# Kernel tuning notes

Measured on AMD Instinct MI355X. Metric: run time of the kernel, lower is better.

The kernel has to match this reference:

```python
import jax, jax.numpy as jnp
import numpy as np
import math

S, B, H, NH = 2048, 1, 4096, 32
D = H // NH  # 128 head dim


def rotate_half(x):
    x1, x2 = x[..., : x.shape[-1] // 2], x[..., x.shape[-1] // 2 :]
    return jnp.concatenate((-x2, x1), axis=-1)


def setup_inputs() -> dict:
    key = jax.random.key(0)
    k1, k2, k3, k4, k5 = jax.random.split(key, 5)
    hidden_states = jax.random.normal(k1, (S, B, H), dtype=jnp.float32)
    position_ids = jnp.broadcast_to(jnp.arange(S, dtype=jnp.int32)[None, :], (B, S))
    # causal mask: True = masked (upper triangle above diagonal)
    attention_mask = jnp.triu(jnp.ones((S, S), dtype=bool), k=1)[None, None]
    W_qkv = jax.random.normal(k2, (H, 3 * H), dtype=jnp.float32) * 0.02
    b_qkv = jax.random.normal(k3, (3 * H,), dtype=jnp.float32) * 0.02
    W_dense = jax.random.normal(k4, (H, H), dtype=jnp.float32) * 0.02
    b_dense = jax.random.normal(k5, (H,), dtype=jnp.float32) * 0.02
    return {
        "hidden_states": hidden_states,
        "position_ids": position_ids,
        "attention_mask": attention_mask,
        "W_qkv": W_qkv,
        "b_qkv": b_qkv,
        "W_dense": W_dense,
        "b_dense": b_dense,
        "layer_id": 27,
    }


def reference(hidden_states, position_ids, attention_mask, W_qkv, b_qkv, W_dense, b_dense, layer_id):
    s, b, h = hidden_states.shape
    nh, d = NH, D
    # QKV projection: [s, b, 3h] -> [s, b, nh, 3d] -> split
    mixed = hidden_states @ W_qkv + b_qkv
    mixed = mixed.reshape(s, b, nh, 3 * d)
    q, k, v = jnp.split(mixed, 3, axis=-1)  # each [s, b, nh, d]
    # rotary embedding indexed by position_ids (transposed to [s, b])
    pos = position_ids.T  # [s, b]
    inv_freq = 1.0 / (10000.0 ** (jnp.arange(0, d, 2, dtype=jnp.float32) / d))
    freqs = pos[..., None].astype(jnp.float32) * inv_freq  # [s, b, d/2]
    emb = jnp.concatenate((freqs, freqs), axis=-1)  # [s, b, d]
    cos = jnp.cos(emb)[:, :, None, :]  # [s, b, 1, d]
    sin = jnp.sin(emb)[:, :, None, :]
    q = q * cos + rotate_half(q) * sin
    k = k * cos + rotate_half(k) * sin
    # attention with per-layer scaling coeff (cancels in softmax except mask fill)
    coeff = jnp.float32(layer_id + 1)
    q_scaled = q / (math.sqrt(d) * coeff)
    scores = jnp.einsum("sbnd,tbnd->bnst", q_scaled, k)  # [b, nh, s, s]
    scores = jnp.where(attention_mask, jnp.float32(-10000.0), scores) * coeff
    probs = jax.nn.softmax(scores, axis=-1)
    ctx = jnp.einsum("bnst,tbnd->sbnd", probs, v).reshape(s, b, h)
    out = ctx @ W_dense + b_dense
    return out
```

## Files before the change

### kernel.cpp

```cpp
#include <hip/hip_runtime.h>

#define S_LEN 2048
#define HID   4096
#define NHEAD 32
#define DHEAD 128
#define H3    12288

typedef __attribute__((ext_vector_type(8))) __bf16 bf16x8;
typedef __attribute__((ext_vector_type(4))) __bf16 bf16x4;
typedef __attribute__((ext_vector_type(4))) float  f32x4;
typedef __attribute__((ext_vector_type(16))) float f32x16;

__device__ __forceinline__ void gl_lds16(const void* g, void* l) {
  __builtin_amdgcn_global_load_lds(
      (const __attribute__((address_space(1))) void*)g,
      (__attribute__((address_space(3))) void*)l, 16, 0, 0);
}

__global__ void cvt_f32_bf16(const float* __restrict__ in, __bf16* __restrict__ out, int n4) {
  int i = blockIdx.x * blockDim.x + threadIdx.x;
  if (i >= n4) return;
  float4 v = ((const float4*)in)[i];
  bf16x4 o;
  o.x = (__bf16)v.x; o.y = (__bf16)v.y; o.z = (__bf16)v.z; o.w = (__bf16)v.w;
  ((bf16x4*)out)[i] = o;
}

__global__ void transpose_cvt(const float* __restrict__ in, __bf16* __restrict__ out, int R, int C) {
  __shared__ float t[64][65];
  const int tid = threadIdx.x;
  const int r0 = blockIdx.y * 64, c0 = blockIdx.x * 64;
#pragma unroll
  for (int p = 0; p < 4; ++p) {
    int r = p * 16 + (tid >> 4);
    int c4 = (tid & 15) * 4;
    float4 v = *(const float4*)(in + (size_t)(r0 + r) * C + c0 + c4);
    t[r][c4] = v.x; t[r][c4 + 1] = v.y; t[r][c4 + 2] = v.z; t[r][c4 + 3] = v.w;
  }
  __syncthreads();
#pragma unroll
  for (int p = 0; p < 4; ++p) {
    int c = p * 16 + (tid >> 4);
    int rg = (tid & 15) * 4;
    bf16x4 o;
    o.x = (__bf16)t[rg][c]; o.y = (__bf16)t[rg + 1][c];
    o.z = (__bf16)t[rg + 2][c]; o.w = (__bf16)t[rg + 3][c];
    *(bf16x4*)(out + (size_t)(c0 + c) * R + r0 + rg) = o;
  }
}

__global__ void rope_kernel(__bf16* __restrict__ q, __bf16* __restrict__ k,
                            const int* __restrict__ pos) {
  int idx = blockIdx.x * 256 + threadIdx.x;
  int j = idx & 63;
  int hs = idx >> 6;
  int s = hs & (S_LEN - 1);
  float p = (float)pos[s];
  float invf = __expf(-(float)j * (9.210340371976184f / 64.f));
  float a = p * invf;
  float c, sn;
  __sincosf(a, &sn, &c);
  const float SC = 0.08838834764831845f;
  size_t base = (size_t)hs * 128;
  float x1 = (float)q[base + j], x2 = (float)q[base + j + 64];
  q[base + j]      = (__bf16)((x1 * c - x2 * sn) * SC);
  q[base + j + 64] = (__bf16)((x2 * c + x1 * sn) * SC);
  x1 = (float)k[base + j]; x2 = (float)k[base + j + 64];
  k[base + j]      = (__bf16)(x1 * c - x2 * sn);
  k[base + j + 64] = (__bf16)(x2 * c + x1 * sn);
}

__global__ __launch_bounds__(256, 2)
void gemm_dense(const __bf16* __restrict__ A, const __bf16* __restrict__ BT,
                const float* __restrict__ bias, int K,
                float* __restrict__ outf) {
  const int tid = threadIdx.x;
  const int lane = tid & 63;
  const int wave = tid >> 6;
  const int bm = blockIdx.x * 128;
  const int bn = blockIdx.y * 128;

  __shared__ char lds[2][32768];

  f32x4 acc[4][4] = {};

  const int wm = (wave >> 1) * 64;
  const int wn = (wave & 1) * 64;

  const int sr = tid >> 3;
  const int sc = (tid & 7) * 16;
  const int scs = sc ^ ((sr & 7) << 4);

  const char* Arow = (const char*)(A + (size_t)(bm + sr) * K) + scs;
  const char* Brow = (const char*)(BT + (size_t)(bn + sr) * K) + scs;

  const int NT = K >> 6;

  auto stage = [&](int t) {
    const char* a_src = Arow + (size_t)t * 128;
    const char* b_src = Brow + (size_t)t * 128;
    char* a_dst = lds[t & 1] + wave * 1024;
    char* b_dst = lds[t & 1] + 16384 + wave * 1024;
#pragma unroll
    for (int i = 0; i < 4; ++i) {
      gl_lds16(a_src + (size_t)i * 32 * K * 2, a_dst + i * 4096);
      gl_lds16(b_src + (size_t)i * 32 * K * 2, b_dst + i * 4096);
    }
  };

  stage(0);
  __syncthreads();
  for (int t = 0; t < NT; ++t) {
    if (t + 1 < NT) stage(t + 1);
    const char* Ab = lds[t & 1];
    const char* Bb = lds[t & 1] + 16384;
#pragma unroll
    for (int kk = 0; kk < 2; ++kk) {
      bf16x8 af[4], bfr[4];
#pragma unroll
      for (int m = 0; m < 4; ++m) {
        int row = wm + m * 16 + (lane & 15);
        int cb = (kk * 64 + ((lane >> 4) << 4)) ^ ((row & 7) << 4);
        af[m] = *(const bf16x8*)(Ab + row * 128 + cb);
      }
#pragma unroll
      for (int n = 0; n < 4; ++n) {
        int row = wn + n * 16 + (lane & 15);
        int cb = (kk * 64 + ((lane >> 4) << 4)) ^ ((row & 7) << 4);
        bfr[n] = *(const bf16x8*)(Bb + row * 128 + cb);
      }
#pragma unroll
      for (int m = 0; m < 4; ++m)
#pragma unroll
        for (int n = 0; n < 4; ++n)
          acc[m][n] = __builtin_amdgcn_mfma_f32_16x16x32_bf16(af[m], bfr[n], acc[m][n], 0, 0, 0);
    }
    __syncthreads();
  }

  const int rbase = (lane >> 4) << 2;
  const int cl = lane & 15;
#pragma unroll
  for (int n = 0; n < 4; ++n) {
    const int col = bn + wn + n * 16 + cl;
    const float bv = bias[col];
#pragma unroll
    for (int m = 0; m < 4; ++m) {
      const int srow = bm + wm + m * 16 + rbase;
#pragma unroll
      for (int r = 0; r < 4; ++r)
        outf[(size_t)(srow + r) * HID + col] = acc[m][n][r] + bv;
    }
  }
}

template <int EPI>
__global__ __launch_bounds__(256, 2)
void gemm32(const __bf16* __restrict__ A, const __bf16* __restrict__ BT,
            const float* __restrict__ bias, int K,
            __bf16* __restrict__ outq, __bf16* __restrict__ outk,
            __bf16* __restrict__ outvt) {
  const int tid = threadIdx.x;
  const int lane = tid & 63;
  const int wave = tid >> 6;
  const int bm = blockIdx.x * 256;
  const int bn = blockIdx.y * 128;

  __shared__ char lds[49152];
  char* Ab = lds;
  char* Bb = lds + 32768;

  f32x16 acc[4][2] = {};

  const int wm = (wave >> 1) * 128;
  const int wn = (wave & 1) * 64;
  const int l31 = lane & 31;
  const int hi = lane >> 5;

  const int sr = tid >> 3;
  const int scb = ((tid & 7) * 16) ^ ((sr & 7) << 4);
  const int K2 = K * 2;
  const char* Arow = (const char*)A + (size_t)(bm + sr) * K2 + scb;
  const char* Brow = (const char*)BT + (size_t)(bn + sr) * K2 + scb;

  for (int k0 = 0; k0 < K; k0 += 64) {
    const char* a_src = Arow + (size_t)k0 * 2;
    const char* b_src = Brow + (size_t)k0 * 2;
    char* a_dst = Ab + wave * 1024;
    char* b_dst = Bb + wave * 1024;
#pragma unroll
    for (int i = 0; i < 8; ++i)
      gl_lds16(a_src + (size_t)i * 32 * K2, a_dst + i * 4096);
#pragma unroll
    for (int i = 0; i < 4; ++i)
      gl_lds16(b_src + (size_t)i * 32 * K2, b_dst + i * 4096);
    __syncthreads();
#pragma unroll
    for (int kk = 0; kk < 4; ++kk) {
      const int cbase = kk * 32 + (hi << 4);
      bf16x8 af[4], bfr[2];
#pragma unroll
      for (int m = 0; m < 4; ++m) {
        const int row = wm + m * 32 + l31;
        af[m] = *(const bf16x8*)(Ab + row * 128 + (cbase ^ ((row & 7) << 4)));
      }
#pragma unroll
      for (int n = 0; n < 2; ++n) {
        const int row = wn + n * 32 + l31;
        bfr[n] = *(const bf16x8*)(Bb + row * 128 + (cbase ^ ((row & 7) << 4)));
      }
#pragma unroll
      for (int m = 0; m < 4; ++m)
#pragma unroll
        for (int n = 0; n < 2; ++n)
          acc[m][n] = __builtin_amdgcn_mfma_f32_32x32x16_bf16(af[m], bfr[n], acc[m][n], 0, 0, 0);
    }
    __syncthreads();
  }

  const int route = (bn >> 7) % 3;
  const int head = bn / 384;
#pragma unroll
  for (int n = 0; n < 2; ++n) {
    const int d = wn + n * 32 + l31;
    const float bv = bias[bn + d];
#pragma unroll
    for (int m = 0; m < 4; ++m) {
      if (route == 2) {
#pragma unroll
        for (int qd = 0; qd < 4; ++qd) {
          const int srow = bm + wm + m * 32 + qd * 8 + (hi << 2);
          bf16x4 o;
          o.x = (__bf16)(acc[m][n][qd * 4 + 0] + bv);
          o.y = (__bf16)(acc[m][n][qd * 4 + 1] + bv);
          o.z = (__bf16)(acc[m][n][qd * 4 + 2] + bv);
          o.w = (__bf16)(acc[m][n][qd * 4 + 3] + bv);
          *(bf16x4*)(outvt + ((size_t)head * 128 + d) * S_LEN + srow) = o;
        }
      } else {
        __bf16* dst = (route == 0 ? outq : outk) + (size_t)head * S_LEN * 128;
#pragma unroll
        for (int r = 0; r < 16; ++r) {
          const int srow = bm + wm + m * 32 + (r & 3) + 8 * (r >> 2) + (hi << 2);
          dst[(size_t)srow * 128 + d] = (__bf16)(acc[m][n][r] + bv);
        }
      }
    }
  }
}

__global__ __launch_bounds__(256, 2)
void attn_kernel(const __bf16* __restrict__ q, const __bf16* __restrict__ k,
                 const __bf16* __restrict__ vt, __bf16* __restrict__ ctx) {
  const int p = blockIdx.x, h = blockIdx.y;
  const int tid = threadIdx.x, lane = tid & 63, wave = tid >> 6;
  __shared__ char Kd[2][16384];
  __shared__ char Vd[2][16384];
  __shared__ __bf16 Ps[4][16 * 64];
  char* Pb = (char*)(Ps[wave]);

  const __bf16* qh = q + (size_t)h * S_LEN * 128;
  const __bf16* kh = k + (size_t)h * S_LEN * 128;
  const __bf16* vh = vt + (size_t)h * 128 * S_LEN;

  const int cl = lane & 15, rbase = (lane >> 4) << 2;

  const int krow = tid >> 4, kcol = (tid & 15) * 16;
  const int kcs = kcol ^ ((krow & 7) << 4);
  const int vrow = tid >> 3, vcol = (tid & 7) * 16;
  const int vcs = vcol ^ ((vrow & 7) << 4);

  auto stage_kv = [&](int j) {
    {
      const char* src = (const char*)(kh + (size_t)(j * 64 + krow) * 128) + kcs;
      char* dst = Kd[j & 1] + wave * 1024;
#pragma unroll
      for (int i = 0; i < 4; ++i)
        gl_lds16(src + (size_t)i * 16 * 256, dst + i * 4096);
    }
    {
      const char* src = (const char*)(vh + (size_t)vrow * S_LEN + j * 64) + vcs;
      char* dst = Vd[j & 1] + wave * 1024;
#pragma unroll
      for (int i = 0; i < 4; ++i)
        gl_lds16(src + (size_t)i * 32 * (S_LEN * 2), dst + i * 4096);
    }
  };

  for (int half = 0; half < 2; ++half) {
    const int qt = half ? (31 - p) : p;
    const int qrow0 = qt * 64 + wave * 16;

    bf16x8 qf[4];
#pragma unroll
    for (int kk = 0; kk < 4; ++kk)
      qf[kk] = *(const bf16x8*)(qh + (size_t)(qrow0 + cl) * 128 + kk * 32 + ((lane >> 4) << 3));

    f32x4 oacc[8] = {};
    float mrow[4], lrow[4];
#pragma unroll
    for (int r = 0; r < 4; ++r) { mrow[r] = -1e30f; lrow[r] = 0.f; }

    const int nt = qt + 1;
    stage_kv(0);
    __syncthreads();

    for (int j = 0; j < nt; ++j) {
      if (j + 1 < nt) stage_kv(j + 1);
      const char* Kb = Kd[j & 1];
      const char* Vb = Vd[j & 1];

      f32x4 sacc[4] = {};
#pragma unroll
      for (int kk = 0; kk < 4; ++kk) {
        bf16x8 bk[4];
#pragma unroll
        for (int n = 0; n < 4; ++n) {
          int row = n * 16 + cl;
          int cb = (kk * 64 + ((lane >> 4) << 4)) ^ ((row & 7) << 4);
          bk[n] = *(const bf16x8*)(Kb + row * 256 + cb);
        }
#pragma unroll
        for (int n = 0; n < 4; ++n)
          sacc[n] = __builtin_amdgcn_mfma_f32_16x16x32_bf16(qf[kk], bk[n], sacc[n], 0, 0, 0);
      }

      float pmax[4];
#pragma unroll
      for (int r = 0; r < 4; ++r) pmax[r] = -1e30f;
      if (j == qt) {
#pragma unroll
        for (int n = 0; n < 4; ++n) {
          const int col = n * 16 + cl;
#pragma unroll
          for (int r = 0; r < 4; ++r) {
            const int row = wave * 16 + rbase + r;
            float sv = (col > row) ? -1e30f : sacc[n][r];
            sacc[n][r] = sv;
            pmax[r] = fmaxf(pmax[r], sv);
          }
        }
      } else {
#pragma unroll
        for (int n = 0; n < 4; ++n)
#pragma unroll
          for (int r = 0; r < 4; ++r)
            pmax[r] = fmaxf(pmax[r], sacc[n][r]);
      }
#pragma unroll
      for (int xm = 1; xm < 16; xm <<= 1)
#pragma unroll
        for (int r = 0; r < 4; ++r)
          pmax[r] = fmaxf(pmax[r], __shfl_xor(pmax[r], xm, 64));

      const bool okd = (pmax[0] <= mrow[0] + 8.f) && (pmax[1] <= mrow[1] + 8.f) &&
                       (pmax[2] <= mrow[2] + 8.f) && (pmax[3] <= mrow[3] + 8.f);
      if (__all(okd)) {
#pragma unroll
        for (int r = 0; r < 4; ++r) {
          float psum = 0.f;
#pragma unroll
          for (int n = 0; n < 4; ++n) {
            float pe = __expf(sacc[n][r] - mrow[r]);
            sacc[n][r] = pe;
            psum += pe;
          }
#pragma unroll
          for (int xm = 1; xm < 16; xm <<= 1)
            psum += __shfl_xor(psum, xm, 64);
          lrow[r] += psum;
        }
      } else {
#pragma unroll
        for (int r = 0; r < 4; ++r) {
          const float mnew = fmaxf(mrow[r], pmax[r]);
          const float alpha = __expf(mrow[r] - mnew);
          mrow[r] = mnew;
          float psum = 0.f;
#pragma unroll
          for (int n = 0; n < 4; ++n) {
            float pe = __expf(sacc[n][r] - mnew);
            sacc[n][r] = pe;
            psum += pe;
          }
#pragma unroll
          for (int xm = 1; xm < 16; xm <<= 1)
            psum += __shfl_xor(psum, xm, 64);
          lrow[r] = lrow[r] * alpha + psum;
#pragma unroll
          for (int nd = 0; nd < 8; ++nd)
            oacc[nd][r] *= alpha;
        }
      }

#pragma unroll
      for (int n = 0; n < 4; ++n) {
        const int colb = (n * 16 + cl) * 2;
#pragma unroll
        for (int r = 0; r < 4; ++r) {
          const int row = rbase + r;
          *(__bf16*)(Pb + row * 128 + (colb ^ ((row & 7) << 4))) = (__bf16)sacc[n][r];
        }
      }

#pragma unroll
      for (int kk = 0; kk < 2; ++kk) {
        bf16x8 pa, bv[8];
        {
          int row = cl;
          int cb = (kk * 64 + ((lane >> 4) << 4)) ^ ((row & 7) << 4);
          pa = *(const bf16x8*)(Pb + row * 128 + cb);
        }
#pragma unroll
        for (int nd = 0; nd < 8; ++nd) {
          int row = nd * 16 + cl;
          int cb = (kk * 64 + ((lane >> 4) << 4)) ^ ((row & 7) << 4);
          bv[nd] = *(const bf16x8*)(Vb + row * 128 + cb);
        }
#pragma unroll
        for (int nd = 0; nd < 8; ++nd)
          oacc[nd] = __builtin_amdgcn_mfma_f32_16x16x32_bf16(pa, bv[nd], oacc[nd], 0, 0, 0);
      }
      __syncthreads();
    }

#pragma unroll
    for (int nd = 0; nd < 8; ++nd) {
      const int d = nd * 16 + cl;
#pragma unroll
      for (int r = 0; r < 4; ++r) {
        const int srow = qrow0 + rbase + r;
        ctx[(size_t)srow * HID + h * 128 + d] = (__bf16)(oacc[nd][r] / lrow[r]);
      }
    }
  }
}

extern "C" void kernel_launch(void* const* d_in, const int* in_sizes, int n_in,
                              void* d_out, int out_size, void* d_ws, size_t ws_size,
                              hipStream_t stream) {
  const float* hs = (const float*)d_in[0];
  const int* pos = (const int*)d_in[1];
  const float* wqkv = (const float*)d_in[3];
  const float* bqkv = (const float*)d_in[4];
  const float* wd = (const float*)d_in[5];
  const float* bd = (const float*)d_in[6];
  float* out = (float*)d_out;

  char* ws = (char*)d_ws;
  const size_t MB = 1024ull * 1024ull;
  if (ws_size < 160 * MB) return;
  __bf16* wT  = (__bf16*)(ws);
  __bf16* xb  = (__bf16*)(ws + 96 * MB);
  __bf16* qb_ = (__bf16*)(ws + 112 * MB);
  __bf16* kb_ = (__bf16*)(ws + 128 * MB);
  __bf16* vtb = (__bf16*)(ws + 144 * MB);

  cvt_f32_bf16<<<8192, 256, 0, stream>>>(hs, xb, 2097152);
  transpose_cvt<<<dim3(192, 64), 256, 0, stream>>>(wqkv, wT, 4096, 12288);
  gemm32<0><<<dim3(8, 96), 256, 0, stream>>>(xb, wT, bqkv, 4096, qb_, kb_, vtb);
  rope_kernel<<<16384, 256, 0, stream>>>(qb_, kb_, pos);
  transpose_cvt<<<dim3(64, 64), 256, 0, stream>>>(wd, wT, 4096, 4096);
  attn_kernel<<<dim3(16, 32), 256, 0, stream>>>(qb_, kb_, vtb, xb);
  gemm_dense<<<dim3(16, 32), 256, 0, stream>>>(xb, wT, bd, 4096, out);
}
```

Baseline: 461.2 us.

## Share K/V tile loads between paired query tiles in one causal sweep

Instead of processing the two query tiles (p and 31-p) one after another, each with its own K/V staging pass, the kernel now walks K/V tiles once up to the larger query tile. Each staged tile feeds both query tiles' online-softmax updates while j is within the smaller tile's range. This removes the duplicated K/V global-to-LDS traffic for the first p+1 tiles and one pipeline restart. In exchange it doubles the live accumulator and Q-fragment registers, which may lower occupancy or cause spills. The shared P buffer is reused by both process calls within an iteration, which is safe only because each wave writes and reads its own region in program order.

New measurement: 648.1 us. 1.41x slower.

```diff
diff --git a/kernel.cpp b/kernel.cpp
--- a/kernel.cpp
+++ b/kernel.cpp
@@ -287,151 +287,159 @@
     }
   };
 
-  for (int half = 0; half < 2; ++half) {
-    const int qt = half ? (31 - p) : p;
-    const int qrow0 = qt * 64 + wave * 16;
-
-    bf16x8 qf[4];
-#pragma unroll
-    for (int kk = 0; kk < 4; ++kk)
-      qf[kk] = *(const bf16x8*)(qh + (size_t)(qrow0 + cl) * 128 + kk * 32 + ((lane >> 4) << 3));
-
-    f32x4 oacc[8] = {};
-    float mrow[4], lrow[4];
-#pragma unroll
-    for (int r = 0; r < 4; ++r) { mrow[r] = -1e30f; lrow[r] = 0.f; }
-
-    const int nt = qt + 1;
-    stage_kv(0);
+  const int qtA = p, qtB = 31 - p;
+
+  bf16x8 qfA[4], qfB[4];
+  {
+    const int rA = qtA * 64 + wave * 16 + cl;
+    const int rB = qtB * 64 + wave * 16 + cl;
+#pragma unroll
+    for (int kk = 0; kk < 4; ++kk) {
+      qfA[kk] = *(const bf16x8*)(qh + (size_t)rA * 128 + kk * 32 + ((lane >> 4) << 3));
+      qfB[kk] = *(const bf16x8*)(qh + (size_t)rB * 128 + kk * 32 + ((lane >> 4) << 3));
+    }
+  }
+
+  f32x4 oA[8] = {}, oB[8] = {};
+  float mA[4], lA[4], mB[4], lB[4];
+#pragma unroll
+  for (int r = 0; r < 4; ++r) { mA[r] = -1e30f; lA[r] = 0.f; mB[r] = -1e30f; lB[r] = 0.f; }
+
+  auto process = [&](const char* Kb, const char* Vb, const bf16x8* qf,
+                     f32x4* oacc, float* mrow, float* lrow, int j, int qt) {
+    f32x4 sacc[4] = {};
+#pragma unroll
+    for (int kk = 0; kk < 4; ++kk) {
+      bf16x8 bk[4];
+#pragma unroll
+      for (int n = 0; n < 4; ++n) {
+        int row = n * 16 + cl;
+        int cb = (kk * 64 + ((lane >> 4) << 4)) ^ ((row & 7) << 4);
+        bk[n] = *(const bf16x8*)(Kb + row * 256 + cb);
+      }
+#pragma unroll
+      for (int n = 0; n < 4; ++n)
+        sacc[n] = __builtin_amdgcn_mfma_f32_16x16x32_bf16(qf[kk], bk[n], sacc[n], 0, 0, 0);
+    }
+
+    float pmax[4];
+#pragma unroll
+    for (int r = 0; r < 4; ++r) pmax[r] = -1e30f;
+    if (j == qt) {
+#pragma unroll
+      for (int n = 0; n < 4; ++n) {
+        const int col = n * 16 + cl;
+#pragma unroll
+        for (int r = 0; r < 4; ++r) {
+          const int row = wave * 16 + rbase + r;
+          float sv = (col > row) ? -1e30f : sacc[n][r];
+          sacc[n][r] = sv;
+          pmax[r] = fmaxf(pmax[r], sv);
+        }
+      }
+    } else {
+#pragma unroll
+      for (int n = 0; n < 4; ++n)
+#pragma unroll
+        for (int r = 0; r < 4; ++r)
+          pmax[r] = fmaxf(pmax[r], sacc[n][r]);
+    }
+#pragma unroll
+    for (int xm = 1; xm < 16; xm <<= 1)
+#pragma unroll
+      for (int r = 0; r < 4; ++r)
+        pmax[r] = fmaxf(pmax[r], __shfl_xor(pmax[r], xm, 64));
+
+    const bool okd = (pmax[0] <= mrow[0] + 8.f) && (pmax[1] <= mrow[1] + 8.f) &&
+                     (pmax[2] <= mrow[2] + 8.f) && (pmax[3] <= mrow[3] + 8.f);
+    if (__all(okd)) {
+#pragma unroll
+      for (int r = 0; r < 4; ++r) {
+        float psum = 0.f;
+#pragma unroll
+        for (int n = 0; n < 4; ++n) {
+          float pe = __expf(sacc[n][r] - mrow[r]);
+          sacc[n][r] = pe;
+          psum += pe;
+        }
+#pragma unroll
+        for (int xm = 1; xm < 16; xm <<= 1)
+          psum += __shfl_xor(psum, xm, 64);
+        lrow[r] += psum;
+      }
+    } else {
+#pragma unroll
+      for (int r = 0; r < 4; ++r) {
+        const float mnew = fmaxf(mrow[r], pmax[r]);
+        const float alpha = __expf(mrow[r] - mnew);
+        mrow[r] = mnew;
+        float psum = 0.f;
+#pragma unroll
+        for (int n = 0; n < 4; ++n) {
+          float pe = __expf(sacc[n][r] - mnew);
+          sacc[n][r] = pe;
+          psum += pe;
+        }
+#pragma unroll
+        for (int xm = 1; xm < 16; xm <<= 1)
+          psum += __shfl_xor(psum, xm, 64);
+        lrow[r] = lrow[r] * alpha + psum;
+#pragma unroll
+        for (int nd = 0; nd < 8; ++nd)
+          oacc[nd][r] *= alpha;
+      }
+    }
+
+#pragma unroll
+    for (int n = 0; n < 4; ++n) {
+      const int colb = (n * 16 + cl) * 2;
+#pragma unroll
+      for (int r = 0; r < 4; ++r) {
+        const int row = rbase + r;
+        *(__bf16*)(Pb + row * 128 + (colb ^ ((row & 7) << 4))) = (__bf16)sacc[n][r];
+      }
+    }
+
+#pragma unroll
+    for (int kk = 0; kk < 2; ++kk) {
+      bf16x8 pa, bv[8];
+      {
+        int row = cl;
+        int cb = (kk * 64 + ((lane >> 4) << 4)) ^ ((row & 7) << 4);
+        pa = *(const bf16x8*)(Pb + row * 128 + cb);
+      }
+#pragma unroll
+      for (int nd = 0; nd < 8; ++nd) {
+        int row = nd * 16 + cl;
+        int cb = (kk * 64 + ((lane >> 4) << 4)) ^ ((row & 7) << 4);
+        bv[nd] = *(const bf16x8*)(Vb + row * 128 + cb);
+      }
+#pragma unroll
+      for (int nd = 0; nd < 8; ++nd)
+        oacc[nd] = __builtin_amdgcn_mfma_f32_16x16x32_bf16(pa, bv[nd], oacc[nd], 0, 0, 0);
+    }
+  };
+
+  stage_kv(0);
+  __syncthreads();
+  for (int j = 0; j <= qtB; ++j) {
+    if (j < qtB) stage_kv(j + 1);
+    const char* Kb = Kd[j & 1];
+    const char* Vb = Vd[j & 1];
+    process(Kb, Vb, qfB, oB, mB, lB, j, qtB);
+    if (j <= qtA) process(Kb, Vb, qfA, oA, mA, lA, j, qtA);
     __syncthreads();
-
-    for (int j = 0; j < nt; ++j) {
-      if (j + 1 < nt) stage_kv(j + 1);
-      const char* Kb = Kd[j & 1];
-      const char* Vb = Vd[j & 1];
-
-      f32x4 sacc[4] = {};
-#pragma unroll
-      for (int kk = 0; kk < 4; ++kk) {
-        bf16x8 bk[4];
-#pragma unroll
-        for (int n = 0; n < 4; ++n) {
-          int row = n * 16 + cl;
-          int cb = (kk * 64 + ((lane >> 4) << 4)) ^ ((row & 7) << 4);
-          bk[n] = *(const bf16x8*)(Kb + row * 256 + cb);
-        }
-#pragma unroll
-        for (int n = 0; n < 4; ++n)
-          sacc[n] = __builtin_amdgcn_mfma_f32_16x16x32_bf16(qf[kk], bk[n], sacc[n], 0, 0, 0);
-      }
-
-      float pmax[4];
-#pragma unroll
-      for (int r = 0; r < 4; ++r) pmax[r] = -1e30f;
-      if (j == qt) {
-#pragma unroll
-        for (int n = 0; n < 4; ++n) {
-          const int col = n * 16 + cl;
-#pragma unroll
-          for (int r = 0; r < 4; ++r) {
-            const int row = wave * 16 + rbase + r;
-            float sv = (col > row) ? -1e30f : sacc[n][r];
-            sacc[n][r] = sv;
-            pmax[r] = fmaxf(pmax[r], sv);
-          }
-        }
-      } else {
-#pragma unroll
-        for (int n = 0; n < 4; ++n)
-#pragma unroll
-          for (int r = 0; r < 4; ++r)
-            pmax[r] = fmaxf(pmax[r], sacc[n][r]);
-      }
-#pragma unroll
-      for (int xm = 1; xm < 16; xm <<= 1)
-#pragma unroll
-        for (int r = 0; r < 4; ++r)
-          pmax[r] = fmaxf(pmax[r], __shfl_xor(pmax[r], xm, 64));
-
-      const bool okd = (pmax[0] <= mrow[0] + 8.f) && (pmax[1] <= mrow[1] + 8.f) &&
-                       (pmax[2] <= mrow[2] + 8.f) && (pmax[3] <= mrow[3] + 8.f);
-      if (__all(okd)) {
-#pragma unroll
-        for (int r = 0; r < 4; ++r) {
-          float psum = 0.f;
-#pragma unroll
-          for (int n = 0; n < 4; ++n) {
-            float pe = __expf(sacc[n][r] - mrow[r]);
-            sacc[n][r] = pe;
-            psum += pe;
-          }
-#pragma unroll
-          for (int xm = 1; xm < 16; xm <<= 1)
-            psum += __shfl_xor(psum, xm, 64);
-          lrow[r] += psum;
-        }
-      } else {
-#pragma unroll
-        for (int r = 0; r < 4; ++r) {
-          const float mnew = fmaxf(mrow[r], pmax[r]);
-          const float alpha = __expf(mrow[r] - mnew);
-          mrow[r] = mnew;
-          float psum = 0.f;
-#pragma unroll
-          for (int n = 0; n < 4; ++n) {
-            float pe = __expf(sacc[n][r] - mnew);
-            sacc[n][r] = pe;
-            psum += pe;
-          }
-#pragma unroll
-          for (int xm = 1; xm < 16; xm <<= 1)
-            psum += __shfl_xor(psum, xm, 64);
-          lrow[r] = lrow[r] * alpha + psum;
-#pragma unroll
-          for (int nd = 0; nd < 8; ++nd)
-            oacc[nd][r] *= alpha;
-        }
-      }
-
-#pragma unroll
-      for (int n = 0; n < 4; ++n) {
-        const int colb = (n * 16 + cl) * 2;
-#pragma unroll
-        for (int r = 0; r < 4; ++r) {
-          const int row = rbase + r;
-          *(__bf16*)(Pb + row * 128 + (colb ^ ((row & 7) << 4))) = (__bf16)sacc[n][r];
-        }
-      }
-
-#pragma unroll
-      for (int kk = 0; kk < 2; ++kk) {
-        bf16x8 pa, bv[8];
-        {
-          int row = cl;
-          int cb = (kk * 64 + ((lane >> 4) << 4)) ^ ((row & 7) << 4);
-          pa = *(const bf16x8*)(Pb + row * 128 + cb);
-        }
-#pragma unroll
-        for (int nd = 0; nd < 8; ++nd) {
-          int row = nd * 16 + cl;
-          int cb = (kk * 64 + ((lane >> 4) << 4)) ^ ((row & 7) << 4);
-          bv[nd] = *(const bf16x8*)(Vb + row * 128 + cb);
-        }
-#pragma unroll
-        for (int nd = 0; nd < 8; ++nd)
-          oacc[nd] = __builtin_amdgcn_mfma_f32_16x16x32_bf16(pa, bv[nd], oacc[nd], 0, 0, 0);
-      }
-      __syncthreads();
-    }
-
-#pragma unroll
-    for (int nd = 0; nd < 8; ++nd) {
-      const int d = nd * 16 + cl;
-#pragma unroll
-      for (int r = 0; r < 4; ++r) {
-        const int srow = qrow0 + rbase + r;
-        ctx[(size_t)srow * HID + h * 128 + d] = (__bf16)(oacc[nd][r] / lrow[r]);
-      }
+  }
+
+#pragma unroll
+  for (int nd = 0; nd < 8; ++nd) {
+    const int d = nd * 16 + cl;
+#pragma unroll
+    for (int r = 0; r < 4; ++r) {
+      const int srowA = qtA * 64 + wave * 16 + rbase + r;
+      const int srowB = qtB * 64 + wave * 16 + rbase + r;
+      ctx[(size_t)srowA * HID + h * 128 + d] = (__bf16)(oA[nd][r] / lA[r]);
+      ctx[(size_t)srowB * HID + h * 128 + d] = (__bf16)(oB[nd][r] / lB[r]);
     }
   }
 }
```
